# Kernel tuning notes

Measured on AMD Instinct MI355X. Metric: run time of the kernel, lower is better.

Reference implementation:

```python
import jax, jax.numpy as jnp
import numpy as np

EPS = 1e-5


def _conv(x, w, b, pad):
    # x: [N,C,H,W], w: [O,I,kh,kw]
    y = jax.lax.conv_general_dilated(
        x, w, window_strides=(1, 1), padding=[(pad, pad), (pad, pad)],
        dimension_numbers=("NCHW", "OIHW", "NCHW"))
    return y + b[None, :, None, None]


def _bn(x, gamma, beta, mean, var):
    scale = gamma / jnp.sqrt(var + EPS)
    return x * scale[None, :, None, None] + (beta - mean * scale)[None, :, None, None]


def _unfold3x3(x):
    # Matches F.unfold(x, kernel_size=3, padding=1).view(N, C*9, H, W):
    # channel-major layout, i.e. out channel index = c*9 + (ki*3 + kj).
    N, C, H, W = x.shape
    xp = jnp.pad(x, ((0, 0), (0, 0), (1, 1), (1, 1)))
    patches = jnp.stack(
        [xp[:, :, i:i + H, j:j + W] for i in range(3) for j in range(3)],
        axis=2)  # [N, C, 9, H, W]
    return patches.reshape(N, C * 9, H, W)


def setup_inputs() -> dict:
    key = jax.random.key(0)
    ks = jax.random.split(key, 8)
    N, C, H, W = 4, 64, 64, 512
    C9 = 9 * C
    s = lambda fan: 1.0 / np.sqrt(fan)
    inp = {
        "xyz": jax.random.normal(ks[0], (N, 3, H, W), jnp.float32),
        "new_xyz": jax.random.normal(ks[1], (N, 3, H, W), jnp.float32),
        "feature": jax.random.normal(ks[2], (N, C, H, W), jnp.float32),
        "w_att": jax.random.normal(ks[3], (C9, 3, 7, 7), jnp.float32) * s(3 * 49),
        "b_att": jnp.zeros((C9,), jnp.float32),
        "bn_att_gamma": jnp.ones((C9,), jnp.float32),
        "bn_att_beta": jnp.zeros((C9,), jnp.float32),
        "bn_att_mean": jnp.zeros((C9,), jnp.float32),
        "bn_att_var": jnp.ones((C9,), jnp.float32),
        "w1": jax.random.normal(ks[4], (C, C9, 1, 1), jnp.float32) * s(C9),
        "b1": jnp.zeros((C,), jnp.float32),
        "bn1_gamma": jnp.ones((C,), jnp.float32),
        "bn1_beta": jnp.zeros((C,), jnp.float32),
        "bn1_mean": jnp.zeros((C,), jnp.float32),
        "bn1_var": jnp.ones((C,), jnp.float32),
        "w2": jax.random.normal(ks[5], (C, C, 3, 3), jnp.float32) * s(C * 9),
        "b2": jnp.zeros((C,), jnp.float32),
        "bn2_gamma": jnp.ones((C,), jnp.float32),
        "bn2_beta": jnp.zeros((C,), jnp.float32),
        "bn2_mean": jnp.zeros((C,), jnp.float32),
        "bn2_var": jnp.ones((C,), jnp.float32),
    }
    return inp


def reference(xyz, new_xyz, feature,
              w_att, b_att, bn_att_gamma, bn_att_beta, bn_att_mean, bn_att_var,
              w1, b1, bn1_gamma, bn1_beta, bn1_mean, bn1_var,
              w2, b2, bn2_gamma, bn2_beta, bn2_mean, bn2_var):
    # unfold neighborhood expand: [N, 9C, H, W]
    new_feature = _unfold3x3(feature)
    # sigmoid attention gate from xyz coords
    attention = jax.nn.sigmoid(
        _bn(_conv(new_xyz, w_att, b_att, pad=3),
            bn_att_gamma, bn_att_beta, bn_att_mean, bn_att_var))
    new_feature = new_feature * attention
    # position_mlp_2: 1x1 conv reduce -> BN -> ReLU -> 3x3 conv -> BN -> ReLU
    h = jax.nn.relu(_bn(_conv(new_feature, w1, b1, pad=0),
                        bn1_gamma, bn1_beta, bn1_mean, bn1_var))
    h = jax.nn.relu(_bn(_conv(h, w2, b2, pad=1),
                        bn2_gamma, bn2_beta, bn2_mean, bn2_var))
    fuse_feature = h + feature
    # original returns (xyz, new_xyz, fuse_feature); xyz/new_xyz are pass-through
    return fuse_feature
```

## Files before the change

kernel.cpp:

```cpp
#include <hip/hip_runtime.h>

#define EPSB 1e-5f

typedef __bf16 bf16x8 __attribute__((ext_vector_type(8)));
typedef float f32x4 __attribute__((ext_vector_type(4)));
typedef float f32x16 __attribute__((ext_vector_type(16)));

__device__ __forceinline__ unsigned short bfc(float v) {
  __bf16 h = (__bf16)v;
  return __builtin_bit_cast(unsigned short, h);
}
__device__ __forceinline__ unsigned int pk2(float a, float b) {
  return (unsigned int)bfc(a) | ((unsigned int)bfc(b) << 16);
}
__device__ __forceinline__ float sigm(float x) {
  float e = __builtin_amdgcn_exp2f(-x * 1.4426950408889634f);
  return __builtin_amdgcn_rcpf(1.0f + e);
}

__global__ void prep_kernel(
    const float* __restrict__ w_att, const float* __restrict__ b_att,
    const float* __restrict__ gA, const float* __restrict__ beA,
    const float* __restrict__ mA, const float* __restrict__ vA,
    const float* __restrict__ w1, const float* __restrict__ b1,
    const float* __restrict__ g1, const float* __restrict__ be1,
    const float* __restrict__ m1, const float* __restrict__ v1,
    const float* __restrict__ w2, const float* __restrict__ b2,
    const float* __restrict__ g2, const float* __restrict__ be2,
    const float* __restrict__ m2, const float* __restrict__ v2,
    unsigned short* __restrict__ wAe, unsigned short* __restrict__ w1e,
    unsigned short* __restrict__ w2e, float* __restrict__ bias1,
    float* __restrict__ bias2)
{
  int i = blockIdx.x * 256 + threadIdx.x;
  if (i < 576 * 160) {
    int rp = i / 160, k = i - rp * 160;
    int kk = rp >> 6, cc = rp & 63;
    int o = cc * 9 + kk;
    float s = gA[o] * rsqrtf(vA[o] + EPSB);
    float v = 0.f;
    if (k < 147) {
      int c = k / 49, rem = k - c * 49, ki = rem / 7, kj = rem - ki * 7;
      v = w_att[(o * 3 + c) * 49 + ki * 7 + kj] * s;
    } else if (k == 147) {
      v = b_att[o] * s + beA[o] - mA[o] * s;
    }
    wAe[i] = bfc(v);
    return;
  }
  i -= 576 * 160;
  if (i < 64 * 576) {
    int o = i / 576, kp = i - o * 576;
    int kk = kp >> 6, cc = kp & 63;
    float s = g1[o] * rsqrtf(v1[o] + EPSB);
    w1e[i] = bfc(w1[o * 576 + cc * 9 + kk] * s);
    return;
  }
  i -= 64 * 576;
  if (i < 64 * 576) {
    int o = i / 576, r = i - o * 576, kk = r >> 6, c = r & 63;
    float s = g2[o] * rsqrtf(v2[o] + EPSB);
    w2e[i] = bfc(w2[(o * 64 + c) * 9 + kk] * s);
    return;
  }
  i -= 64 * 576;
  if (i < 64) {
    float s = g1[i] * rsqrtf(v1[i] + EPSB);
    bias1[i] = b1[i] * s + be1[i] - m1[i] * s;
  } else if (i < 128) {
    int o = i - 64;
    float s = g2[o] * rsqrtf(v2[o] + EPSB);
    bias2[o] = b2[o] * s + be2[o] - m2[o] * s;
  }
}

__global__ __launch_bounds__(512, 4) void k12_kernel(
    const float* __restrict__ new_xyz, const float* __restrict__ feature,
    const unsigned short* __restrict__ wAe, const unsigned short* __restrict__ w1e,
    const float* __restrict__ bias1, unsigned short* __restrict__ h1g)
{
  __shared__ __align__(16) unsigned char smem[77824];
  unsigned short* B1p  = (unsigned short*)smem;
  unsigned short* B2p  = (unsigned short*)(smem + 43008);
  unsigned short* xyzb = B2p;
  int* lut             = (int*)(smem + 43008 + 6256);

  const int bx = blockIdx.x;
  const int x0 = bx * 128;
  const int y  = blockIdx.y;
  const int n  = blockIdx.z;
  const int tid = threadIdx.x;
  const int lane = tid & 63;
  const int wv = tid >> 6;
  const int r16 = lane & 15;
  const int kq = (lane >> 4) & 3;
  const int l32 = lane & 31;
  const int hi = lane >> 5;
  const int wrow = wv & 3, wcol = wv >> 2;
  const int wh = wrow >> 1;
  const bool xedge = (bx == 0) || (bx == 3);

  for (int row = wv; row < 21; row += 8) {
    int c = (row >= 14) ? 2 : (row >= 7 ? 1 : 0);
    int ki = row - c * 7;
    int yy = y + ki - 3;
    bool rowok = (unsigned)yy < 64u;
    unsigned short* dst = xyzb + row * 136;
    if (rowok && !xedge) {
      const float* src = new_xyz + ((n * 3 + c) * 64 + yy) * 512 + (x0 - 3);
      dst[lane] = bfc(src[lane]);
      dst[64 + lane] = bfc(src[64 + lane]);
      if (lane < 6) dst[128 + lane] = bfc(src[128 + lane]);
    } else {
      const float* src = new_xyz + ((n * 3 + c) * 64 + yy) * 512;
#pragma unroll
      for (int seg = 0; seg < 3; ++seg) {
        int xx = lane + seg * 64;
        if (xx < 134) {
          int xg = x0 + xx - 3;
          float v = (rowok && (unsigned)xg < 512u) ? src[xg] : 0.f;
          dst[xx] = bfc(v);
        }
      }
    }
  }
  if (tid < 136) { xyzb[21 * 136 + tid] = 0; xyzb[22 * 136 + tid] = 0x3F80; }
  else if (tid >= 256 && tid < 416) {
    int k = tid - 256;
    int off;
    if (k < 147) { int c = k / 49, rem = k - c * 49, ki = rem / 7, kj = rem - ki * 7; off = (c * 7 + ki) * 136 + kj; }
    else if (k == 147) off = 22 * 136;
    else off = 21 * 136;
    lut[k] = off;
  }
  __syncthreads();

  {
    int p = tid >> 2, q = tid & 3;
    unsigned short* brow = B1p + p * 168;
#pragma unroll
    for (int j = 0; j < 10; ++j) {
      int k = (q * 10 + j) * 4;
      int o0 = lut[k], o1 = lut[k + 1], o2 = lut[k + 2], o3 = lut[k + 3];
      uint2 w;
      w.x = (unsigned int)xyzb[o0 + p] | ((unsigned int)xyzb[o1 + p] << 16);
      w.y = (unsigned int)xyzb[o2 + p] | ((unsigned int)xyzb[o3 + p] << 16);
      *(uint2*)(brow + k) = w;
    }
  }
  __syncthreads();

  const int p64 = 64 * wcol;
  const int ccq = (wrow & 1) * 32;
  const unsigned short* Bp1a = B1p + (p64 + l32) * 168 + hi * 8;
  const unsigned short* Bp1b = Bp1a + 32 * 168;

  f32x4 acc2[4];
#pragma unroll
  for (int i = 0; i < 4; ++i) acc2[i] = {0.f, 0.f, 0.f, 0.f};

#pragma unroll
  for (int c = 0; c < 4; ++c) {
    const int kkA = 2 * c + wh;
    const int di = (kkA >= 6) ? 2 : (kkA >= 3 ? 1 : 0);
    const int dj = kkA - 3 * di;

    const int yy = y + di - 1;
    const bool yok = (unsigned)yy < 64u;
    float fvv[32];
#pragma unroll
    for (int h = 0; h < 2; ++h) {
      const int xg = x0 + p64 + 32 * h + l32 + dj - 1;
      const bool ok = yok && ((unsigned)xg < 512u);
      const float* fbase = feature + (n * 4096 + yy) * 512 + xg;
#pragma unroll
      for (int q = 0; q < 4; ++q) {
        const int c0 = ccq + 8 * q + 4 * hi;
#pragma unroll
        for (int j = 0; j < 4; ++j)
          fvv[16 * h + 4 * q + j] = ok ? fbase[(c0 + j) * 32768] : 0.f;
      }
    }

    f32x16 acc1a, acc1b;
#pragma unroll
    for (int i = 0; i < 16; ++i) { acc1a[i] = 0.f; acc1b[i] = 0.f; }
    const unsigned short* Ap = wAe + (c * 128 + wrow * 32 + l32) * 160 + hi * 8;
#pragma unroll
    for (int j = 0; j < 10; ++j) {
      bf16x8 a  = *(const bf16x8*)(Ap + j * 16);
      bf16x8 ba = *(const bf16x8*)(Bp1a + j * 16);
      bf16x8 bb = *(const bf16x8*)(Bp1b + j * 16);
      acc1a = __builtin_amdgcn_mfma_f32_32x32x16_bf16(a, ba, acc1a, 0, 0, 0);
      acc1b = __builtin_amdgcn_mfma_f32_32x32x16_bf16(a, bb, acc1b, 0, 0, 0);
    }

    bf16x8 a2f[4];
    const unsigned short* A2p = w1e + (16 * wrow + r16) * 576 + c * 128 + kq * 8;
#pragma unroll
    for (int kst = 0; kst < 4; ++kst) a2f[kst] = *(const bf16x8*)(A2p + kst * 32);

#pragma unroll
    for (int h = 0; h < 2; ++h) {
      unsigned short* brow2 = B2p + (p64 + 32 * h + l32) * 136 + wrow * 32;
      const f32x16& a1 = h ? acc1b : acc1a;
#pragma unroll
      for (int q = 0; q < 4; ++q) {
        int r0 = 8 * q + 4 * hi;
        float s0 = sigm(a1[4 * q + 0]) * fvv[16 * h + 4 * q + 0];
        float s1 = sigm(a1[4 * q + 1]) * fvv[16 * h + 4 * q + 1];
        float s2 = sigm(a1[4 * q + 2]) * fvv[16 * h + 4 * q + 2];
        float s3 = sigm(a1[4 * q + 3]) * fvv[16 * h + 4 * q + 3];
        uint2 w; w.x = pk2(s0, s1); w.y = pk2(s2, s3);
        *(uint2*)(brow2 + r0) = w;
      }
    }
    __syncthreads();

#pragma unroll
    for (int kst = 0; kst < 4; ++kst) {
#pragma unroll
      for (int pf = 0; pf < 4; ++pf) {
        bf16x8 b = *(const bf16x8*)(B2p + (p64 + 16 * pf + r16) * 136 + kst * 32 + kq * 8);
        acc2[pf] = __builtin_amdgcn_mfma_f32_16x16x32_bf16(a2f[kst], b, acc2[pf], 0, 0, 0);
      }
    }
    __syncthreads();
  }

  {
    if (wrow < 2) {
      const int yy = y + 1;
      const bool yok = (unsigned)yy < 64u;
      float fvv[32];
#pragma unroll
      for (int h = 0; h < 2; ++h) {
        const int xg = x0 + p64 + 32 * h + l32 + 1;
        const bool ok = yok && ((unsigned)xg < 512u);
        const float* fbase = feature + (n * 4096 + yy) * 512 + xg;
#pragma unroll
        for (int q = 0; q < 4; ++q) {
          const int c0 = ccq + 8 * q + 4 * hi;
#pragma unroll
          for (int j = 0; j < 4; ++j)
            fvv[16 * h + 4 * q + j] = ok ? fbase[(c0 + j) * 32768] : 0.f;
        }
      }
      f32x16 acc1a, acc1b;
#pragma unroll
      for (int i = 0; i < 16; ++i) { acc1a[i] = 0.f; acc1b[i] = 0.f; }
      const unsigned short* Ap = wAe + (512 + wrow * 32 + l32) * 160 + hi * 8;
#pragma unroll
      for (int j = 0; j < 10; ++j) {
        bf16x8 a  = *(const bf16x8*)(Ap + j * 16);
        bf16x8 ba = *(const bf16x8*)(Bp1a + j * 16);
        bf16x8 bb = *(const bf16x8*)(Bp1b + j * 16);
        acc1a = __builtin_amdgcn_mfma_f32_32x32x16_bf16(a, ba, acc1a, 0, 0, 0);
        acc1b = __builtin_amdgcn_mfma_f32_32x32x16_bf16(a, bb, acc1b, 0, 0, 0);
      }
#pragma unroll
      for (int h = 0; h < 2; ++h) {
        unsigned short* brow2 = B2p + (p64 + 32 * h + l32) * 136 + wrow * 32;
        const f32x16& a1 = h ? acc1b : acc1a;
#pragma unroll
        for (int q = 0; q < 4; ++q) {
          int r0 = 8 * q + 4 * hi;
          float s0 = sigm(a1[4 * q + 0]) * fvv[16 * h + 4 * q + 0];
          float s1 = sigm(a1[4 * q + 1]) * fvv[16 * h + 4 * q + 1];
          float s2 = sigm(a1[4 * q + 2]) * fvv[16 * h + 4 * q + 2];
          float s3 = sigm(a1[4 * q + 3]) * fvv[16 * h + 4 * q + 3];
          uint2 w; w.x = pk2(s0, s1); w.y = pk2(s2, s3);
          *(uint2*)(brow2 + r0) = w;
        }
      }
    }
    bf16x8 a2f[2];
    const unsigned short* A2p = w1e + (16 * wrow + r16) * 576 + 512 + kq * 8;
    a2f[0] = *(const bf16x8*)(A2p);
    a2f[1] = *(const bf16x8*)(A2p + 32);
    __syncthreads();
#pragma unroll
    for (int kst = 0; kst < 2; ++kst) {
#pragma unroll
      for (int pf = 0; pf < 4; ++pf) {
        bf16x8 b = *(const bf16x8*)(B2p + (p64 + 16 * pf + r16) * 136 + kst * 32 + kq * 8);
        acc2[pf] = __builtin_amdgcn_mfma_f32_16x16x32_bf16(a2f[kst], b, acc2[pf], 0, 0, 0);
      }
    }
    __syncthreads();
  }

  const int ccb = 16 * wrow + 4 * kq;
  float b1v0 = bias1[ccb], b1v1 = bias1[ccb + 1], b1v2 = bias1[ccb + 2], b1v3 = bias1[ccb + 3];
#pragma unroll
  for (int pf = 0; pf < 4; ++pf) {
    int p = p64 + 16 * pf + r16;
    uint2 w;
    w.x = pk2(fmaxf(acc2[pf][0] + b1v0, 0.f), fmaxf(acc2[pf][1] + b1v1, 0.f));
    w.y = pk2(fmaxf(acc2[pf][2] + b1v2, 0.f), fmaxf(acc2[pf][3] + b1v3, 0.f));
    *(uint2*)(B2p + p * 136 + ccb) = w;
  }
  __syncthreads();
  {
    int p = tid >> 2, c0 = (tid & 3) * 16;
    uint4 v0 = *(const uint4*)(B2p + p * 136 + c0);
    uint4 v1 = *(const uint4*)(B2p + p * 136 + c0 + 8);
    unsigned short* dst = h1g + (((n * 64 + y) * 512) + x0 + p) * 64 + c0;
    *(uint4*)dst = v0;
    *(uint4*)(dst + 8) = v1;
  }
}

__global__ __launch_bounds__(256) void k3_kernel(
    const unsigned short* __restrict__ h1g, const float* __restrict__ feature,
    const unsigned short* __restrict__ w2e, const float* __restrict__ bias2,
    float* __restrict__ out)
{
  __shared__ unsigned short s_h1[3][66][72];

  const int x0 = blockIdx.x * 64;
  const int y  = blockIdx.y;
  const int n  = blockIdx.z;
  const int tid = threadIdx.x;
  const int lane = tid & 63;
  const int wv = tid >> 6;
  const int r16 = lane & 15;
  const int kq = lane >> 4;

  for (int idx = tid; idx < 3 * 66 * 16; idx += 256) {
    int r = idx / (66 * 16), rem = idx - r * 66 * 16, xx = rem >> 4, c0 = (rem & 15) << 2;
    int yy = y + r - 1, xg = x0 + xx - 1;
    uint2 v; v.x = 0u; v.y = 0u;
    if (yy >= 0 && yy < 64 && xg >= 0 && xg < 512)
      v = *(const uint2*)(h1g + (((n * 64 + yy) * 512) + xg) * 64 + c0);
    *(uint2*)(&s_h1[r][xx][c0]) = v;
  }
  __syncthreads();

  f32x4 acc[4];
#pragma unroll
  for (int i = 0; i < 4; ++i) acc[i] = {0.f, 0.f, 0.f, 0.f};

  const unsigned short* Ap = w2e + (16 * wv + r16) * 576 + kq * 8;
#pragma unroll 2
  for (int kst = 0; kst < 18; ++kst) {
    bf16x8 a = *(const bf16x8*)(Ap + kst * 32);
    int kk = kst >> 1, di = kk / 3, dj = kk - di * 3;
    int chalf = (kst & 1) << 5;
#pragma unroll
    for (int pf = 0; pf < 4; ++pf) {
      bf16x8 b = *(const bf16x8*)(&s_h1[di][pf * 16 + r16 + dj][chalf + kq * 8]);
      acc[pf] = __builtin_amdgcn_mfma_f32_16x16x32_bf16(a, b, acc[pf], 0, 0, 0);
    }
  }

#pragma unroll
  for (int pf = 0; pf < 4; ++pf) {
    int p = pf * 16 + r16;
#pragma unroll
    for (int r = 0; r < 4; ++r) {
      int ch = 16 * wv + kq * 4 + r;
      int off = (((n * 64 + ch) * 64) + y) * 512 + x0 + p;
      out[off] = fmaxf(acc[pf][r] + bias2[ch], 0.f) + feature[off];
    }
  }
}

extern "C" void kernel_launch(void* const* d_in, const int* in_sizes, int n_in,
                              void* d_out, int out_size, void* d_ws, size_t ws_size,
                              hipStream_t stream)
{
  const float* new_xyz = (const float*)d_in[1];
  const float* feature = (const float*)d_in[2];
  const float* w_att = (const float*)d_in[3];
  const float* b_att = (const float*)d_in[4];
  const float* gA  = (const float*)d_in[5];
  const float* beA = (const float*)d_in[6];
  const float* mA  = (const float*)d_in[7];
  const float* vA  = (const float*)d_in[8];
  const float* w1  = (const float*)d_in[9];
  const float* b1  = (const float*)d_in[10];
  const float* g1  = (const float*)d_in[11];
  const float* be1 = (const float*)d_in[12];
  const float* m1  = (const float*)d_in[13];
  const float* v1  = (const float*)d_in[14];
  const float* w2  = (const float*)d_in[15];
  const float* b2  = (const float*)d_in[16];
  const float* g2  = (const float*)d_in[17];
  const float* be2 = (const float*)d_in[18];
  const float* m2  = (const float*)d_in[19];
  const float* v2  = (const float*)d_in[20];

  char* ws = (char*)d_ws;
  unsigned short* wAe = (unsigned short*)(ws);
  unsigned short* w1e = (unsigned short*)(ws + 184320);
  unsigned short* w2e = (unsigned short*)(ws + 258048);
  float* bias1 = (float*)(ws + 331776);
  float* bias2 = (float*)(ws + 332032);
  unsigned short* h1g = (unsigned short*)(ws + 335872);

  prep_kernel<<<649, 256, 0, stream>>>(w_att, b_att, gA, beA, mA, vA,
                                       w1, b1, g1, be1, m1, v1,
                                       w2, b2, g2, be2, m2, v2,
                                       wAe, w1e, w2e, bias1, bias2);
  k12_kernel<<<dim3(4, 64, 4), 512, 0, stream>>>(new_xyz, feature, wAe, w1e, bias1, h1g);
  k3_kernel<<<dim3(8, 64, 4), 256, 0, stream>>>(h1g, feature, w2e, bias2, (float*)d_out);
}
```

Baseline: 120.1 us.

## Software-pipeline feature and w1 loads across chunks of the fused attention GEMM

Merges the four main chunks and the tail chunk into one loop and prefetches the next chunk's feature values and w1 fragments into registers before the barrier. The goal is to hide global-load latency behind the attention MFMA and sigmoid work. The first loads are also issued before the initial barrier. This uses more registers, which could lower occupancy or cause spills.

After: 197.8 us. +64.7%, slower.

```diff
diff --git a/kernel.cpp b/kernel.cpp
--- a/kernel.cpp
+++ b/kernel.cpp
@@ -148,108 +148,59 @@
       *(uint2*)(brow + k) = w;
     }
   }
-  __syncthreads();
 
   const int p64 = 64 * wcol;
   const int ccq = (wrow & 1) * 32;
   const unsigned short* Bp1a = B1p + (p64 + l32) * 168 + hi * 8;
   const unsigned short* Bp1b = Bp1a + 32 * 168;
 
+  auto load_fvv = [&](int kk, float* fv) {
+    int di = (kk >= 6) ? 2 : (kk >= 3 ? 1 : 0);
+    int dj = kk - 3 * di;
+    int yy = y + di - 1;
+    bool yok = (unsigned)yy < 64u;
+#pragma unroll
+    for (int h = 0; h < 2; ++h) {
+      int xg = x0 + p64 + 32 * h + l32 + dj - 1;
+      bool ok = yok && ((unsigned)xg < 512u);
+      const float* fbase = feature + (n * 4096 + yy) * 512 + xg;
+#pragma unroll
+      for (int q = 0; q < 4; ++q) {
+        int c0 = ccq + 8 * q + 4 * hi;
+#pragma unroll
+        for (int j = 0; j < 4; ++j)
+          fv[16 * h + 4 * q + j] = ok ? fbase[(c0 + j) * 32768] : 0.f;
+      }
+    }
+  };
+  auto load_a2f = [&](int c, int cnt, bf16x8* dst) {
+    const unsigned short* A2p = w1e + (16 * wrow + r16) * 576 + c * 128 + kq * 8;
+#pragma unroll
+    for (int kst = 0; kst < 4; ++kst)
+      if (kst < cnt) dst[kst] = *(const bf16x8*)(A2p + kst * 32);
+  };
+
+  float fvv[32];
+  bf16x8 a2f[4];
+  load_fvv(wh, fvv);
+  load_a2f(0, 4, a2f);
+
   f32x4 acc2[4];
 #pragma unroll
   for (int i = 0; i < 4; ++i) acc2[i] = {0.f, 0.f, 0.f, 0.f};
 
-#pragma unroll
-  for (int c = 0; c < 4; ++c) {
-    const int kkA = 2 * c + wh;
-    const int di = (kkA >= 6) ? 2 : (kkA >= 3 ? 1 : 0);
-    const int dj = kkA - 3 * di;
-
-    const int yy = y + di - 1;
-    const bool yok = (unsigned)yy < 64u;
-    float fvv[32];
-#pragma unroll
-    for (int h = 0; h < 2; ++h) {
-      const int xg = x0 + p64 + 32 * h + l32 + dj - 1;
-      const bool ok = yok && ((unsigned)xg < 512u);
-      const float* fbase = feature + (n * 4096 + yy) * 512 + xg;
-#pragma unroll
-      for (int q = 0; q < 4; ++q) {
-        const int c0 = ccq + 8 * q + 4 * hi;
-#pragma unroll
-        for (int j = 0; j < 4; ++j)
-          fvv[16 * h + 4 * q + j] = ok ? fbase[(c0 + j) * 32768] : 0.f;
-      }
-    }
+  __syncthreads();
+
+#pragma unroll
+  for (int c = 0; c <= 4; ++c) {
+    const bool active = (c < 4) || (wrow < 2);
 
     f32x16 acc1a, acc1b;
 #pragma unroll
     for (int i = 0; i < 16; ++i) { acc1a[i] = 0.f; acc1b[i] = 0.f; }
-    const unsigned short* Ap = wAe + (c * 128 + wrow * 32 + l32) * 160 + hi * 8;
-#pragma unroll
-    for (int j = 0; j < 10; ++j) {
-      bf16x8 a  = *(const bf16x8*)(Ap + j * 16);
-      bf16x8 ba = *(const bf16x8*)(Bp1a + j * 16);
-      bf16x8 bb = *(const bf16x8*)(Bp1b + j * 16);
-      acc1a = __builtin_amdgcn_mfma_f32_32x32x16_bf16(a, ba, acc1a, 0, 0, 0);
-      acc1b = __builtin_amdgcn_mfma_f32_32x32x16_bf16(a, bb, acc1b, 0, 0, 0);
-    }
-
-    bf16x8 a2f[4];
-    const unsigned short* A2p = w1e + (16 * wrow + r16) * 576 + c * 128 + kq * 8;
-#pragma unroll
-    for (int kst = 0; kst < 4; ++kst) a2f[kst] = *(const bf16x8*)(A2p + kst * 32);
-
-#pragma unroll
-    for (int h = 0; h < 2; ++h) {
-      unsigned short* brow2 = B2p + (p64 + 32 * h + l32) * 136 + wrow * 32;
-      const f32x16& a1 = h ? acc1b : acc1a;
-#pragma unroll
-      for (int q = 0; q < 4; ++q) {
-        int r0 = 8 * q + 4 * hi;
-        float s0 = sigm(a1[4 * q + 0]) * fvv[16 * h + 4 * q + 0];
-        float s1 = sigm(a1[4 * q + 1]) * fvv[16 * h + 4 * q + 1];
-        float s2 = sigm(a1[4 * q + 2]) * fvv[16 * h + 4 * q + 2];
-        float s3 = sigm(a1[4 * q + 3]) * fvv[16 * h + 4 * q + 3];
-        uint2 w; w.x = pk2(s0, s1); w.y = pk2(s2, s3);
-        *(uint2*)(brow2 + r0) = w;
-      }
-    }
-    __syncthreads();
-
-#pragma unroll
-    for (int kst = 0; kst < 4; ++kst) {
-#pragma unroll
-      for (int pf = 0; pf < 4; ++pf) {
-        bf16x8 b = *(const bf16x8*)(B2p + (p64 + 16 * pf + r16) * 136 + kst * 32 + kq * 8);
-        acc2[pf] = __builtin_amdgcn_mfma_f32_16x16x32_bf16(a2f[kst], b, acc2[pf], 0, 0, 0);
-      }
-    }
-    __syncthreads();
-  }
-
-  {
-    if (wrow < 2) {
-      const int yy = y + 1;
-      const bool yok = (unsigned)yy < 64u;
-      float fvv[32];
-#pragma unroll
-      for (int h = 0; h < 2; ++h) {
-        const int xg = x0 + p64 + 32 * h + l32 + 1;
-        const bool ok = yok && ((unsigned)xg < 512u);
-        const float* fbase = feature + (n * 4096 + yy) * 512 + xg;
-#pragma unroll
-        for (int q = 0; q < 4; ++q) {
-          const int c0 = ccq + 8 * q + 4 * hi;
-#pragma unroll
-          for (int j = 0; j < 4; ++j)
-            fvv[16 * h + 4 * q + j] = ok ? fbase[(c0 + j) * 32768] : 0.f;
-        }
-      }
-      f32x16 acc1a, acc1b;
-#pragma unroll
-      for (int i = 0; i < 16; ++i) { acc1a[i] = 0.f; acc1b[i] = 0.f; }
-      const unsigned short* Ap = wAe + (512 + wrow * 32 + l32) * 160 + hi * 8;
+    if (active) {
+      const int rowb = (c < 4) ? (c * 128 + wrow * 32) : (512 + wrow * 32);
+      const unsigned short* Ap = wAe + (rowb + l32) * 160 + hi * 8;
 #pragma unroll
       for (int j = 0; j < 10; ++j) {
         bf16x8 a  = *(const bf16x8*)(Ap + j * 16);
@@ -274,21 +225,37 @@
         }
       }
     }
-    bf16x8 a2f[2];
-    const unsigned short* A2p = w1e + (16 * wrow + r16) * 576 + 512 + kq * 8;
-    a2f[0] = *(const bf16x8*)(A2p);
-    a2f[1] = *(const bf16x8*)(A2p + 32);
+
+    float fvvN[32];
+    bf16x8 a2fN[4];
+    if (c < 4) {
+      const int kkN = (c + 1 < 4) ? (2 * (c + 1) + wh) : 8;
+      if ((c + 1 < 4) || (wrow < 2)) load_fvv(kkN, fvvN);
+      load_a2f(c + 1, (c + 1 == 4) ? 2 : 4, a2fN);
+    }
+
     __syncthreads();
-#pragma unroll
-    for (int kst = 0; kst < 2; ++kst) {
+
+#pragma unroll
+    for (int kst = 0; kst < 4; ++kst) {
+      if (c == 4 && kst >= 2) break;
 #pragma unroll
       for (int pf = 0; pf < 4; ++pf) {
         bf16x8 b = *(const bf16x8*)(B2p + (p64 + 16 * pf + r16) * 136 + kst * 32 + kq * 8);
         acc2[pf] = __builtin_amdgcn_mfma_f32_16x16x32_bf16(a2f[kst], b, acc2[pf], 0, 0, 0);
       }
     }
-    __syncthreads();
-  }
+
+    if (c < 4) __syncthreads();
+
+    if (c < 4) {
+#pragma unroll
+      for (int j = 0; j < 32; ++j) fvv[j] = fvvN[j];
+#pragma unroll
+      for (int j = 0; j < 4; ++j) a2f[j] = a2fN[j];
+    }
+  }
+  __syncthreads();
 
   const int ccb = 16 * wrow + 4 * kq;
   float b1v0 = bias1[ccb], b1v1 = bias1[ccb + 1], b1v2 = bias1[ccb + 2], b1v3 = bias1[ccb + 3];
```
